# Kernel optimization log

Measured on AMD Instinct MI355X. Metric: run time of the kernel, lower is better.

## Reference

```python
import jax, jax.numpy as jnp
import numpy as np

B, CIN, COUT, T, J = 64, 128, 128, 128, 25
EPS = 1e-5  # BatchNorm2d default eps


def setup_inputs() -> dict:
    key = jax.random.key(0)
    k = jax.random.split(key, 5)
    x = jax.random.normal(k[0], (B, CIN, T, J), jnp.float32)
    adj = jax.random.normal(k[1], (J, J), jnp.float32) / np.sqrt(J).astype(np.float32)
    Wk = jax.random.normal(k[2], (COUT, CIN), jnp.float32) / np.sqrt(CIN).astype(np.float32)
    Wq = jax.random.normal(k[3], (COUT, CIN), jnp.float32) / np.sqrt(CIN).astype(np.float32)
    Ws = jax.random.normal(k[4], (COUT, CIN), jnp.float32) / np.sqrt(CIN).astype(np.float32)
    return {
        "x": x, "adj": adj,
        "Wk": Wk, "bk": jnp.zeros((COUT,), jnp.float32),
        "Wq": Wq, "bq": jnp.zeros((COUT,), jnp.float32),
        "Ws": Ws, "bs": jnp.zeros((COUT,), jnp.float32),
        "gamma": jnp.ones((COUT,), jnp.float32),
        "beta": jnp.zeros((COUT,), jnp.float32),
        "run_mean": jnp.zeros((COUT,), jnp.float32),
        "run_var": jnp.ones((COUT,), jnp.float32),
        "alpha": jnp.ones((1,), jnp.float32),
    }


def reference(x, adj, Wk, bk, Wq, bq, Ws, bs, gamma, beta, run_mean, run_var, alpha):
    # static graph conv: aggregate over joints with the shared adjacency
    static = jnp.einsum('bctj,jk->bctk', x, adj)              # [B,Cin,T,J]
    # 1x1 conv == channel matmul
    static_feat = jnp.einsum('oc,bctj->botj', Ws, static) + bs[None, :, None, None]  # [B,Cout,T,J]
    # temporal mean pooling, then key/query 1x1 convs
    x_t = x.mean(axis=2)                                      # [B,Cin,J]
    kk = jnp.einsum('oc,bcj->boj', Wk, x_t) + bk[None, :, None]  # [B,Cout,J]
    qq = jnp.einsum('oc,bcj->boj', Wq, x_t) + bq[None, :, None]  # [B,Cout,J]
    # attention-style dynamic adjacency: softmax(q^T k / sqrt(Cout)) over last axis
    scale = jnp.sqrt(jnp.asarray(kk.shape[1], x.dtype))
    scores = jnp.einsum('bcj,bck->bjk', qq, kk) / scale       # [B,J,J]
    dyn = jax.nn.softmax(scores, axis=-1)                     # [B,J,J]
    # original expands dyn to (B*T, Cout, J, J); same math without materialization:
    dyn_feat = jnp.einsum('bctj,bjk->bctk', static_feat, dyn)  # [B,Cout,T,J]
    out = static_feat + alpha[0] * dyn_feat
    # BatchNorm2d in inference mode (running stats), then ReLU
    inv = gamma[None, :, None, None] * jax.lax.rsqrt(run_var[None, :, None, None] + EPS)
    out = (out - run_mean[None, :, None, None]) * inv + beta[None, :, None, None]
    return jax.nn.relu(out)
```

## Files before the change

kernel.cpp:

```cpp
#include <hip/hip_runtime.h>

#define B_ 64
#define C_ 128
#define T_ 128
#define J_ 25
#define PIT 136
#define XP 40
#define GP 136
#define TT 4

typedef unsigned short ushort_t;
typedef __attribute__((ext_vector_type(8))) unsigned short ushort8;
typedef __attribute__((ext_vector_type(4))) unsigned short ushort4_t;
typedef __attribute__((ext_vector_type(8))) _Float16 half8;
typedef __attribute__((ext_vector_type(4))) float f32x4;
typedef float f32x4u __attribute__((ext_vector_type(4), aligned(4)));
typedef unsigned short ushort8u __attribute__((ext_vector_type(8), aligned(2)));

__device__ __forceinline__ float bf2f(ushort_t u) {
  unsigned int v = ((unsigned int)u) << 16;
  return __builtin_bit_cast(float, v);
}
__device__ __forceinline__ ushort_t f2bf(float f) {
  unsigned int u = __builtin_bit_cast(unsigned int, f);
  u += 0x7FFFu + ((u >> 16) & 1u);
  return (ushort_t)(u >> 16);
}
__device__ __forceinline__ ushort_t f2h_bits(float f) {
  _Float16 h = (_Float16)f;
  return __builtin_bit_cast(ushort_t, h);
}
__device__ __forceinline__ float h2f(ushort_t u) {
  return (float)__builtin_bit_cast(_Float16, u);
}
__device__ __forceinline__ half8 cvt_bf8_h8(ushort8 u) {
  half8 r;
#pragma unroll
  for (int i = 0; i < 8; ++i) r[i] = (_Float16)bf2f(u[i]);
  return r;
}
__device__ __forceinline__ float ldv(const void* p, long i, int isf32) {
  return isf32 ? ((const float*)p)[i] : bf2f(((const ushort_t*)p)[i]);
}
__device__ __forceinline__ half8 ld8h(const void* p, long i, int isf32) {
  half8 r;
  if (isf32) {
    const float* f = (const float*)p + i;
    f32x4 v0 = *(const f32x4*)f;
    f32x4 v1 = *(const f32x4*)(f + 4);
#pragma unroll
    for (int k = 0; k < 4; ++k) {
      r[k] = (_Float16)v0[k];
      r[4 + k] = (_Float16)v1[k];
    }
  } else {
    ushort8 u = *(const ushort8*)((const ushort_t*)p + i);
    r = cvt_bf8_h8(u);
  }
  return r;
}

__device__ __forceinline__ int detect_isf32(const void* p, int tid) {
  const ushort_t* u = (const ushort_t*)p;
  float a = fabsf(bf2f(u[2 * (tid & 63)]));
  int ok = (a > 1e-4f && a < 64.f) ? 1 : 0;
  unsigned long long m = __ballot(ok);
  return (__popcll(m) > 32) ? 0 : 1;
}

__global__ __launch_bounds__(256) void k_mean(const void* __restrict__ x,
                                              ushort_t* __restrict__ xt) {
  const int bc = blockIdx.x;
  const int b = bc >> 7, c = bc & 127;
  const long base = (long)bc * 3200;
  const int tid = threadIdx.x;
  const int isf32 = detect_isf32((const ushort_t*)x + base, tid);
  __shared__ float pl[3200];
  __shared__ float red[8][32];
  if (isf32) {
    const f32x4* src = (const f32x4*)((const float*)x + base);
    for (int i = tid; i < 800; i += 256) *(f32x4*)&pl[i * 4] = src[i];
  } else {
    const ushort8* src = (const ushort8*)((const ushort_t*)x + base);
    for (int i = tid; i < 400; i += 256) {
      ushort8 u = src[i];
      f32x4 v0, v1;
#pragma unroll
      for (int r = 0; r < 4; ++r) {
        v0[r] = bf2f(u[r]);
        v1[r] = bf2f(u[4 + r]);
      }
      *(f32x4*)&pl[i * 8] = v0;
      *(f32x4*)&pl[i * 8 + 4] = v1;
    }
  }
  __syncthreads();
  const int j = tid & 31, g = tid >> 5;
  float s = 0.f;
  if (j < J_) {
#pragma unroll
    for (int i = 0; i < 16; ++i) s += pl[(g * 16 + i) * 25 + j];
  }
  red[g][j] = s;
  __syncthreads();
  if (tid < 32) {
    float tot = 0.f;
#pragma unroll
    for (int gg = 0; gg < 8; ++gg) tot += red[gg][tid];
    if (tid < J_) xt[b * 4096 + tid * 128 + c] = f2h_bits(tot * (1.0f / 128.0f));
  }
}

__global__ __launch_bounds__(512) void k_attn(
    const ushort_t* __restrict__ xt, const void* __restrict__ adj,
    const void* __restrict__ Wk, const void* __restrict__ bk,
    const void* __restrict__ Wq, const void* __restrict__ bq,
    const void* __restrict__ alphap, ushort_t* __restrict__ fkws,
    float* __restrict__ sws) {
  const int b = blockIdx.x;
  const int tid = threadIdx.x;
  const int isf32 = detect_isf32(Wk, tid);
  const int wv = tid >> 6, lane = tid & 63, lrow = lane & 15, quad = lane >> 4;
  const int mg = wv >> 2, wvv = wv & 3;
  const float alpha = ldv(alphap, 0, isf32);

  __shared__ __align__(16) ushort_t xtT[32 * PIT];
  __shared__ __align__(16) ushort_t kkT[32 * PIT];
  __shared__ __align__(16) ushort_t qqT[32 * PIT];
  __shared__ float sc[32 * 33];
  __shared__ float adjL[25 * 26];

  for (int idx = tid; idx < 32 * 17; idx += 512) {
    int r = idx / 17, c8 = idx % 17;
    ushort8 v = {};
    if (r < J_ && c8 < 16) v = *(const ushort8*)&xt[b * 4096 + r * 128 + c8 * 8];
    *(ushort8*)&xtT[r * PIT + c8 * 8] = v;
  }
  for (int idx = tid; idx < 625; idx += 512)
    adjL[(idx / 25) * 26 + (idx % 25)] = ldv(adj, idx, isf32);
  __syncthreads();

  {
    const void* W = mg ? Wq : Wk;
    const void* bias = mg ? bq : bk;
    ushort_t* dstT = mg ? qqT : kkT;
    f32x4 acc[2][2] = {};
    for (int ks = 0; ks < 4; ++ks) {
      half8 bfr[2];
#pragma unroll
      for (int jt = 0; jt < 2; ++jt)
        bfr[jt] = *(const half8*)&xtT[(jt * 16 + lrow) * PIT + ks * 32 + quad * 8];
#pragma unroll
      for (int ot = 0; ot < 2; ++ot) {
        int o = (2 * wvv + ot) * 16 + lrow;
        half8 afr = ld8h(W, o * 128 + ks * 32 + quad * 8, isf32);
#pragma unroll
        for (int jt = 0; jt < 2; ++jt)
          acc[ot][jt] = __builtin_amdgcn_mfma_f32_16x16x32_f16(afr, bfr[jt],
                                                               acc[ot][jt], 0, 0, 0);
      }
    }
#pragma unroll
    for (int ot = 0; ot < 2; ++ot) {
      int obase = (2 * wvv + ot) * 16 + quad * 4;
#pragma unroll
      for (int jt = 0; jt < 2; ++jt) {
        int j = jt * 16 + lrow;
        ushort_t pack[4];
#pragma unroll
        for (int r = 0; r < 4; ++r)
          pack[r] = f2h_bits(acc[ot][jt][r] + ldv(bias, obase + r, isf32));
        *(ushort4_t*)&dstT[j * PIT + obase] = *(ushort4_t*)pack;
      }
    }
  }
  __syncthreads();

  if (wv < 4) {
    const int mt = wv >> 1, nt = wv & 1;
    f32x4 acc = {};
    for (int ks = 0; ks < 4; ++ks) {
      half8 afr = *(const half8*)&qqT[(mt * 16 + lrow) * PIT + ks * 32 + quad * 8];
      half8 bfr = *(const half8*)&kkT[(nt * 16 + lrow) * PIT + ks * 32 + quad * 8];
      acc = __builtin_amdgcn_mfma_f32_16x16x32_f16(afr, bfr, acc, 0, 0, 0);
    }
    const float rs = 0.08838834764831845f;
#pragma unroll
    for (int r = 0; r < 4; ++r)
      sc[(mt * 16 + quad * 4 + r) * 33 + nt * 16 + lrow] = acc[r] * rs;
  }
  __syncthreads();

  if (tid < J_) {
    float m = -1e30f;
    for (int k = 0; k < J_; ++k) m = fmaxf(m, sc[tid * 33 + k]);
    float sum = 0.f;
    for (int k = 0; k < J_; ++k) {
      float e = expf(sc[tid * 33 + k] - m);
      sc[tid * 33 + k] = e;
      sum += e;
    }
    float inv = 1.f / sum;
    for (int k = 0; k < J_; ++k) sc[tid * 33 + k] *= inv;
  }
  __syncthreads();

  for (int idx = tid; idx < 1280; idx += 512) {
    int k = idx / XP, jj = idx % XP;
    float v = 0.f;
    if (k < J_ && jj < J_) {
      v = adjL[jj * 26 + k];
      float d = 0.f;
      for (int m = 0; m < J_; ++m) d += adjL[jj * 26 + m] * sc[m * 33 + k];
      v += alpha * d;
    }
    fkws[b * 1280 + idx] = f2h_bits(v);
  }
  if (tid < 32) {
    float v = 0.f;
    if (tid < J_) {
      float d = 0.f;
      for (int jj = 0; jj < J_; ++jj) d += sc[jj * 33 + tid];
      v = 1.f + alpha * d;
    }
    sws[b * 32 + tid] = v;
  }
}

#define SM_FK 0
#define SM_GT 2560
#define SM_TOT (2560 + 100 * GP * 2)
__global__ __launch_bounds__(256, 4) void k_main(
    const void* __restrict__ x, const void* __restrict__ Ws,
    const void* __restrict__ bs, const void* __restrict__ gamma,
    const void* __restrict__ beta, const void* __restrict__ rmean,
    const void* __restrict__ rvar, const ushort_t* __restrict__ fkws,
    const float* __restrict__ sws, void* __restrict__ out) {
  const int tid = threadIdx.x;
  const int isf32 = detect_isf32(Ws, tid);
  const int p = blockIdx.x;
  const int idx0 = (p & 7) * 256 + (p >> 3);
  const int b = idx0 >> 5, tb = idx0 & 31, t0 = tb * TT;
  const int wv = tid >> 6, lane = tid & 63, lrow = lane & 15, quad = lane >> 4;

  __shared__ __align__(16) char smem[SM_TOT];
  __shared__ float bnscale[128], bnshift[128], bsv[128], sv[32];
  ushort_t* fk = (ushort_t*)(smem + SM_FK);
  ushort_t* gt = (ushort_t*)(smem + SM_GT);
  ushort_t* outbuf = (ushort_t*)(smem + SM_GT);

  half8 wsf[2][4];
#pragma unroll
  for (int ot = 0; ot < 2; ++ot) {
    int o = (2 * wv + ot) * 16 + lrow;
#pragma unroll
    for (int ks = 0; ks < 4; ++ks)
      wsf[ot][ks] = ld8h(Ws, o * 128 + ks * 32 + quad * 8, isf32);
  }

  for (int i = tid; i < 160; i += 256)
    *(ushort8*)&fk[i * 8] = *(const ushort8*)&fkws[b * 1280 + i * 8];
  if (tid < 32) sv[tid] = sws[b * 32 + tid];
  if (tid < 128) {
    float g = ldv(gamma, tid, isf32), v = ldv(rvar, tid, isf32);
    float scl = g * rsqrtf(v + 1e-5f);
    bnscale[tid] = scl;
    bnshift[tid] = ldv(beta, tid, isf32) - ldv(rmean, tid, isf32) * scl;
    bsv[tid] = ldv(bs, tid, isf32);
  }
  __syncthreads();

  {
    half8 afr[2];
#pragma unroll
    for (int mt = 0; mt < 2; ++mt)
      afr[mt] = *(const half8*)&fk[(mt * 16 + lrow) * XP + quad * 8];
    const float* xf = (const float*)x;
    const ushort_t* xh = (const ushort_t*)x;

    half8 xa[8];
#pragma unroll
    for (int t = 0; t < TT; ++t) {
#pragma unroll
      for (int ci = 0; ci < 2; ++ci) {
        int ct = 2 * wv + ci;
        long pp = (long)b * 409600 + (long)(ct * 16 + lrow) * 3200 + (t0 + t) * 25;
        half8 bfr;
        if (quad < 3) {
          if (isf32) {
            f32x4u v0 = *(const f32x4u*)(xf + pp + quad * 8);
            f32x4u v1 = *(const f32x4u*)(xf + pp + quad * 8 + 4);
#pragma unroll
            for (int r = 0; r < 4; ++r) {
              bfr[r] = (_Float16)v0[r];
              bfr[4 + r] = (_Float16)v1[r];
            }
          } else {
            ushort8u u = *(const ushort8u*)(xh + pp + quad * 8);
#pragma unroll
            for (int r = 0; r < 8; ++r) bfr[r] = (_Float16)bf2f(u[r]);
          }
        } else {
          bfr = (half8){};
          bfr[0] = (_Float16)(isf32 ? xf[pp + 24] : bf2f(xh[pp + 24]));
        }
        xa[t * 2 + ci] = bfr;
      }
    }

#pragma unroll
    for (int t = 0; t < TT; ++t) {
#pragma unroll
      for (int ci = 0; ci < 2; ++ci) {
        int ct = 2 * wv + ci;
        f32x4 accg[2] = {};
#pragma unroll
        for (int mt = 0; mt < 2; ++mt)
          accg[mt] = __builtin_amdgcn_mfma_f32_16x16x32_f16(afr[mt], xa[t * 2 + ci],
                                                            accg[mt], 0, 0, 0);
#pragma unroll
        for (int mt = 0; mt < 2; ++mt)
#pragma unroll
          for (int r = 0; r < 4; ++r) {
            int kk = mt * 16 + quad * 4 + r;
            if (kk < J_)
              gt[(t * 25 + kk) * GP + ct * 16 + lrow] = f2h_bits(accg[mt][r]);
          }
      }
    }
  }
  __syncthreads();

  f32x4 acc[2][7];
#pragma unroll
  for (int ot = 0; ot < 2; ++ot)
#pragma unroll
    for (int nt = 0; nt < 7; ++nt) acc[ot][nt] = (f32x4){};
  for (int ks = 0; ks < 4; ++ks) {
#pragma unroll
    for (int nt = 0; nt < 7; ++nt) {
      half8 bfr = (half8){};
      if (nt < 6 || lrow < 4)
        bfr = *(const half8*)&gt[(nt * 16 + lrow) * GP + ks * 32 + quad * 8];
#pragma unroll
      for (int ot = 0; ot < 2; ++ot)
        acc[ot][nt] = __builtin_amdgcn_mfma_f32_16x16x32_f16(wsf[ot][ks], bfr,
                                                             acc[ot][nt], 0, 0, 0);
    }
  }
  __syncthreads();

#pragma unroll
  for (int nt = 0; nt < 7; ++nt) {
    int n = nt * 16 + lrow;
    if (n < 100) {
      float svk = sv[n % 25];
#pragma unroll
      for (int ot = 0; ot < 2; ++ot) {
        int obase = (2 * wv + ot) * 16 + quad * 4;
#pragma unroll
        for (int r = 0; r < 4; ++r) {
          int o = obase + r;
          float v = acc[ot][nt][r] + bsv[o] * svk;
          v = v * bnscale[o] + bnshift[o];
          outbuf[o * 100 + n] = f2h_bits(fmaxf(v, 0.f));
        }
      }
    }
  }
  __syncthreads();

  {
    const long obase = ((long)(b * 128) * 128 + t0) * 25;
    if (isf32) {
      float* of = (float*)out + obase;
      for (int i2 = tid; i2 < 3200; i2 += 256) {
        int o = i2 / 25, q = i2 % 25;
        ushort4_t u = *(const ushort4_t*)&outbuf[o * 100 + q * 4];
        f32x4 v;
#pragma unroll
        for (int r = 0; r < 4; ++r) v[r] = h2f(u[r]);
        *(f32x4*)(of + (long)o * 3200 + q * 4) = v;
      }
    } else {
      ushort_t* oh = (ushort_t*)out + obase;
      for (int i2 = tid; i2 < 3200; i2 += 256) {
        int o = i2 / 25, q = i2 % 25;
        ushort4_t u = *(const ushort4_t*)&outbuf[o * 100 + q * 4];
        ushort4_t w;
#pragma unroll
        for (int r = 0; r < 4; ++r) w[r] = f2bf(h2f(u[r]));
        *(ushort4_t*)(oh + (long)o * 3200 + q * 4) = w;
      }
    }
  }
}

extern "C" void kernel_launch(void* const* d_in, const int* in_sizes, int n_in,
                              void* d_out, int out_size, void* d_ws, size_t ws_size,
                              hipStream_t stream) {
  const void* x = d_in[0];
  const void* adj = d_in[1];
  const void* Wk = d_in[2];
  const void* bk = d_in[3];
  const void* Wq = d_in[4];
  const void* bq = d_in[5];
  const void* Ws = d_in[6];
  const void* bsp = d_in[7];
  const void* gamma = d_in[8];
  const void* beta = d_in[9];
  const void* rmean = d_in[10];
  const void* rvar = d_in[11];
  const void* alphap = d_in[12];

  char* ws = (char*)d_ws;
  ushort_t* xt = (ushort_t*)ws;
  ushort_t* fkws = (ushort_t*)(ws + 64 * 4096 * 2);
  float* sws = (float*)(ws + 64 * 4096 * 2 + 64 * 1280 * 2);

  k_mean<<<B_ * C_, 256, 0, stream>>>(x, xt);
  k_attn<<<B_, 512, 0, stream>>>(xt, adj, Wk, bk, Wq, bq, alphap, fkws, sws);
  k_main<<<B_ * (T_ / TT), 256, 0, stream>>>(x, Ws, bsp, gamma, beta, rmean, rvar,
                                             fkws, sws, d_out);
}
```

Before: 262.8 us.

## Fuse attention computation into main kernel, recomputing per block

Removes the separate per-batch attention kernel and instead has every main-kernel block recompute k/q projections, softmax scores and the fused adjacency for its batch directly from the temporal-mean buffer. The mean kernel now writes zeros for padded joint rows so the fused kernel can read xt straight from global memory. This drops one launch and the workspace round trip for fkws/sws. In exchange, each of the 32 blocks per batch repeats the attention work, including loading Wk and Wq, which adds redundant compute and memory traffic per block.

Result: slower. 297.1 us (+13.0%).

```diff
diff --git a/kernel.cpp b/kernel.cpp
--- a/kernel.cpp
+++ b/kernel.cpp
@@ -68,10 +68,10 @@
   return (__popcll(m) > 32) ? 0 : 1;
 }
 
-__global__ __launch_bounds__(256) void k_mean(const void* __restrict__ x,
+__global__ __launch_bounds__(256) void k_prep(const void* __restrict__ x,
                                               ushort_t* __restrict__ xt) {
   const int bc = blockIdx.x;
-  const int b = bc >> 7, c = bc & 127;
+  const int b = bc >> 7;
   const long base = (long)bc * 3200;
   const int tid = threadIdx.x;
   const int isf32 = detect_isf32((const ushort_t*)x + base, tid);
@@ -107,52 +107,69 @@
     float tot = 0.f;
 #pragma unroll
     for (int gg = 0; gg < 8; ++gg) tot += red[gg][tid];
-    if (tid < J_) xt[b * 4096 + tid * 128 + c] = f2h_bits(tot * (1.0f / 128.0f));
-  }
-}
-
-__global__ __launch_bounds__(512) void k_attn(
-    const ushort_t* __restrict__ xt, const void* __restrict__ adj,
-    const void* __restrict__ Wk, const void* __restrict__ bk,
-    const void* __restrict__ Wq, const void* __restrict__ bq,
-    const void* __restrict__ alphap, ushort_t* __restrict__ fkws,
-    float* __restrict__ sws) {
-  const int b = blockIdx.x;
+    xt[b * 4096 + tid * 128 + (bc & 127)] =
+        (tid < J_) ? f2h_bits(tot * (1.0f / 128.0f)) : (ushort_t)0;
+  }
+}
+
+#define SM_FK 0
+#define SM_GT 2560
+#define SM_KK 2560
+#define SM_QQ (2560 + 8704)
+#define SM_SC (2560 + 17408)
+#define SM_ADJ (2560 + 21632)
+#define SM_TOT (2560 + 100 * GP * 2)
+__global__ __launch_bounds__(256, 4) void k_fused(
+    const void* __restrict__ x, const ushort_t* __restrict__ xt,
+    const void* __restrict__ adj, const void* __restrict__ Wk,
+    const void* __restrict__ bk, const void* __restrict__ Wq,
+    const void* __restrict__ bq, const void* __restrict__ Ws,
+    const void* __restrict__ bs, const void* __restrict__ gamma,
+    const void* __restrict__ beta, const void* __restrict__ rmean,
+    const void* __restrict__ rvar, const void* __restrict__ alphap,
+    void* __restrict__ out) {
   const int tid = threadIdx.x;
-  const int isf32 = detect_isf32(Wk, tid);
+  const int isf32 = detect_isf32(Ws, tid);
+  const int p = blockIdx.x;
+  const int idx0 = (p & 7) * 256 + (p >> 3);
+  const int b = idx0 >> 5, tb = idx0 & 31, t0 = tb * TT;
   const int wv = tid >> 6, lane = tid & 63, lrow = lane & 15, quad = lane >> 4;
-  const int mg = wv >> 2, wvv = wv & 3;
   const float alpha = ldv(alphap, 0, isf32);
 
-  __shared__ __align__(16) ushort_t xtT[32 * PIT];
-  __shared__ __align__(16) ushort_t kkT[32 * PIT];
-  __shared__ __align__(16) ushort_t qqT[32 * PIT];
-  __shared__ float sc[32 * 33];
-  __shared__ float adjL[25 * 26];
-
-  for (int idx = tid; idx < 32 * 17; idx += 512) {
-    int r = idx / 17, c8 = idx % 17;
-    ushort8 v = {};
-    if (r < J_ && c8 < 16) v = *(const ushort8*)&xt[b * 4096 + r * 128 + c8 * 8];
-    *(ushort8*)&xtT[r * PIT + c8 * 8] = v;
-  }
-  for (int idx = tid; idx < 625; idx += 512)
+  __shared__ __align__(16) char smem[SM_TOT];
+  __shared__ float bnscale[128], bnshift[128], bsv[128], sv[32];
+  ushort_t* fk = (ushort_t*)(smem + SM_FK);
+  ushort_t* gt = (ushort_t*)(smem + SM_GT);
+  ushort_t* outbuf = (ushort_t*)(smem + SM_GT);
+  ushort_t* kkT = (ushort_t*)(smem + SM_KK);
+  ushort_t* qqT = (ushort_t*)(smem + SM_QQ);
+  float* sc = (float*)(smem + SM_SC);
+  float* adjL = (float*)(smem + SM_ADJ);
+
+  for (int idx = tid; idx < 625; idx += 256)
     adjL[(idx / 25) * 26 + (idx % 25)] = ldv(adj, idx, isf32);
-  __syncthreads();
-
-  {
-    const void* W = mg ? Wq : Wk;
-    const void* bias = mg ? bq : bk;
-    ushort_t* dstT = mg ? qqT : kkT;
+  if (tid < 128) {
+    float g = ldv(gamma, tid, isf32), v = ldv(rvar, tid, isf32);
+    float scl = g * rsqrtf(v + 1e-5f);
+    bnscale[tid] = scl;
+    bnshift[tid] = ldv(beta, tid, isf32) - ldv(rmean, tid, isf32) * scl;
+    bsv[tid] = ldv(bs, tid, isf32);
+  }
+
+  for (int mat = 0; mat < 2; ++mat) {
+    const void* W = mat ? Wq : Wk;
+    const void* bias = mat ? bq : bk;
+    ushort_t* dstT = mat ? qqT : kkT;
     f32x4 acc[2][2] = {};
     for (int ks = 0; ks < 4; ++ks) {
       half8 bfr[2];
 #pragma unroll
       for (int jt = 0; jt < 2; ++jt)
-        bfr[jt] = *(const half8*)&xtT[(jt * 16 + lrow) * PIT + ks * 32 + quad * 8];
+        bfr[jt] = *(const half8*)&xt[b * 4096 + (jt * 16 + lrow) * 128 +
+                                     ks * 32 + quad * 8];
 #pragma unroll
       for (int ot = 0; ot < 2; ++ot) {
-        int o = (2 * wvv + ot) * 16 + lrow;
+        int o = (2 * wv + ot) * 16 + lrow;
         half8 afr = ld8h(W, o * 128 + ks * 32 + quad * 8, isf32);
 #pragma unroll
         for (int jt = 0; jt < 2; ++jt)
@@ -162,7 +179,7 @@
     }
 #pragma unroll
     for (int ot = 0; ot < 2; ++ot) {
-      int obase = (2 * wvv + ot) * 16 + quad * 4;
+      int obase = (2 * wv + ot) * 16 + quad * 4;
 #pragma unroll
       for (int jt = 0; jt < 2; ++jt) {
         int j = jt * 16 + lrow;
@@ -176,7 +193,7 @@
   }
   __syncthreads();
 
-  if (wv < 4) {
+  {
     const int mt = wv >> 1, nt = wv & 1;
     f32x4 acc = {};
     for (int ks = 0; ks < 4; ++ks) {
@@ -205,7 +222,7 @@
   }
   __syncthreads();
 
-  for (int idx = tid; idx < 1280; idx += 512) {
+  for (int idx = tid; idx < 1280; idx += 256) {
     int k = idx / XP, jj = idx % XP;
     float v = 0.f;
     if (k < J_ && jj < J_) {
@@ -214,7 +231,7 @@
       for (int m = 0; m < J_; ++m) d += adjL[jj * 26 + m] * sc[m * 33 + k];
       v += alpha * d;
     }
-    fkws[b * 1280 + idx] = f2h_bits(v);
+    fk[idx] = f2h_bits(v);
   }
   if (tid < 32) {
     float v = 0.f;
@@ -223,50 +240,7 @@
       for (int jj = 0; jj < J_; ++jj) d += sc[jj * 33 + tid];
       v = 1.f + alpha * d;
     }
-    sws[b * 32 + tid] = v;
-  }
-}
-
-#define SM_FK 0
-#define SM_GT 2560
-#define SM_TOT (2560 + 100 * GP * 2)
-__global__ __launch_bounds__(256, 4) void k_main(
-    const void* __restrict__ x, const void* __restrict__ Ws,
-    const void* __restrict__ bs, const void* __restrict__ gamma,
-    const void* __restrict__ beta, const void* __restrict__ rmean,
-    const void* __restrict__ rvar, const ushort_t* __restrict__ fkws,
-    const float* __restrict__ sws, void* __restrict__ out) {
-  const int tid = threadIdx.x;
-  const int isf32 = detect_isf32(Ws, tid);
-  const int p = blockIdx.x;
-  const int idx0 = (p & 7) * 256 + (p >> 3);
-  const int b = idx0 >> 5, tb = idx0 & 31, t0 = tb * TT;
-  const int wv = tid >> 6, lane = tid & 63, lrow = lane & 15, quad = lane >> 4;
-
-  __shared__ __align__(16) char smem[SM_TOT];
-  __shared__ float bnscale[128], bnshift[128], bsv[128], sv[32];
-  ushort_t* fk = (ushort_t*)(smem + SM_FK);
-  ushort_t* gt = (ushort_t*)(smem + SM_GT);
-  ushort_t* outbuf = (ushort_t*)(smem + SM_GT);
-
-  half8 wsf[2][4];
-#pragma unroll
-  for (int ot = 0; ot < 2; ++ot) {
-    int o = (2 * wv + ot) * 16 + lrow;
-#pragma unroll
-    for (int ks = 0; ks < 4; ++ks)
-      wsf[ot][ks] = ld8h(Ws, o * 128 + ks * 32 + quad * 8, isf32);
-  }
-
-  for (int i = tid; i < 160; i += 256)
-    *(ushort8*)&fk[i * 8] = *(const ushort8*)&fkws[b * 1280 + i * 8];
-  if (tid < 32) sv[tid] = sws[b * 32 + tid];
-  if (tid < 128) {
-    float g = ldv(gamma, tid, isf32), v = ldv(rvar, tid, isf32);
-    float scl = g * rsqrtf(v + 1e-5f);
-    bnscale[tid] = scl;
-    bnshift[tid] = ldv(beta, tid, isf32) - ldv(rmean, tid, isf32) * scl;
-    bsv[tid] = ldv(bs, tid, isf32);
+    sv[tid] = v;
   }
   __syncthreads();
 
@@ -328,6 +302,15 @@
           }
       }
     }
+  }
+
+  half8 wsf[2][4];
+#pragma unroll
+  for (int ot = 0; ot < 2; ++ot) {
+    int o = (2 * wv + ot) * 16 + lrow;
+#pragma unroll
+    for (int ks = 0; ks < 4; ++ks)
+      wsf[ot][ks] = ld8h(Ws, o * 128 + ks * 32 + quad * 8, isf32);
   }
   __syncthreads();
 
@@ -413,13 +396,10 @@
   const void* rvar = d_in[11];
   const void* alphap = d_in[12];
 
-  char* ws = (char*)d_ws;
-  ushort_t* xt = (ushort_t*)ws;
-  ushort_t* fkws = (ushort_t*)(ws + 64 * 4096 * 2);
-  float* sws = (float*)(ws + 64 * 4096 * 2 + 64 * 1280 * 2);
-
-  k_mean<<<B_ * C_, 256, 0, stream>>>(x, xt);
-  k_attn<<<B_, 512, 0, stream>>>(xt, adj, Wk, bk, Wq, bq, alphap, fkws, sws);
-  k_main<<<B_ * (T_ / TT), 256, 0, stream>>>(x, Ws, bsp, gamma, beta, rmean, rvar,
-                                             fkws, sws, d_out);
-}
+  ushort_t* xt = (ushort_t*)d_ws;
+
+  k_prep<<<B_ * C_, 256, 0, stream>>>(x, xt);
+  k_fused<<<B_ * (T_ / TT), 256, 0, stream>>>(x, xt, adj, Wk, bk, Wq, bq, Ws,
+                                              bsp, gamma, beta, rmean, rvar,
+                                              alphap, d_out);
+}
```
